# Optimization experiments

Hardware: AMD Instinct MI355X
Metric: run time of the kernel (lower is better)

The kernel has to match this reference:

```python
import jax, jax.numpy as jnp
import numpy as np

NEG_INF = -9e15
ALPHA = 0.2  # leaky relu negative slope


def setup_inputs() -> dict:
    key = jax.random.key(0)
    ks = jax.random.split(key, 7)
    B, N, FIN, FOUT = 4, 2048, 512, 128
    inp = {
        "input": jax.random.normal(ks[0], (B, N, FIN), dtype=jnp.float32),
        "W": jax.random.normal(ks[1], (FIN, FOUT), dtype=jnp.float32) * (1.414 / np.sqrt(FIN)),
        "a1": jax.random.normal(ks[2], (FOUT, 1), dtype=jnp.float32) * 0.1,
        "a2": jax.random.normal(ks[3], (FOUT, 1), dtype=jnp.float32) * 0.1,
        "adj": jax.random.randint(ks[4], (B, N, N), 0, 4, dtype=jnp.int32),
        "adj_tree": jax.random.randint(ks[5], (B, N, N), 0, 4, dtype=jnp.int32),
        "d1": 1,
        "d2": 2,
    }
    return inp


def reference(input, W, a1, a2, adj, adj_tree, d1, d2):
    # adj_tree is accepted but unused by the original forward.
    h = jnp.einsum("bnf,fo->bno", input, W)          # [B,N,out]
    t1 = jnp.einsum("bno,ok->bnk", h, a1)            # [B,N,1]
    t2 = jnp.einsum("bno,ok->bnk", h, a2)            # [B,N,1]
    # e[b,i,j] = t1[b,i] + t2[b,j]  (broadcast add, no repeat needed)
    e = jax.nn.leaky_relu(t1 + jnp.swapaxes(t2, 1, 2), negative_slope=ALPHA)
    att = jnp.where(adj == d1, e, NEG_INF)
    att = jnp.where(adj == d2, e, att)
    att = jax.nn.softmax(att, axis=2)
    # dropout is identity in eval mode (training=False)
    h_prime = jnp.einsum("bij,bjo->bio", att, h)     # [B,N,out]
    return h_prime
```

## Files before the change

kernel.cpp:

```cpp
#include <hip/hip_runtime.h>
#include <hip/hip_bf16.h>

#define NN 2048
#define FIN 512
#define FOUT 128
#define NEGV -9e15f
#define ALPHAV 0.2f
#define LOG2E 1.44269504088896340736f

typedef __attribute__((ext_vector_type(8))) short bf16x8;
typedef __attribute__((ext_vector_type(4))) float f32x4;

__device__ __forceinline__ unsigned cvt_pk_bf16(float lo, float hi) {
    unsigned r;
    asm("v_cvt_pk_bf16_f32 %0, %1, %2" : "=v"(r) : "v"(lo), "v"(hi));
    return r;
}

__device__ __forceinline__ unsigned short f32_to_bf16(float f) {
    unsigned int u = __float_as_uint(f);
    unsigned int r = (u + 0x7FFFu + ((u >> 16) & 1u)) >> 16;
    return (unsigned short)r;
}

__global__ void k_wrep(const float* __restrict__ W,
                       unsigned short* __restrict__ whi,
                       unsigned short* __restrict__ wlo) {
    int kt = blockIdx.x >> 3;
    int t_o = blockIdx.x & 7;
    int l = threadIdx.x;
    int lr = l & 15, lg = l >> 4;
    unsigned short vh[8], vl[8];
#pragma unroll
    for (int jj = 0; jj < 8; jj++) {
        float f = W[(size_t)(kt * 32 + lg * 8 + jj) * FOUT + t_o * 16 + lr];
        unsigned short h = f32_to_bf16(f);
        float hf = __uint_as_float(((unsigned)h) << 16);
        vh[jj] = h;
        vl[jj] = f32_to_bf16(f - hf);
    }
    size_t o = ((size_t)(kt * 8 + t_o) * 64 + l) * 8;
    *(uint4*)(whi + o) = *(const uint4*)vh;
    *(uint4*)(wlo + o) = *(const uint4*)vl;
}

__global__ void __launch_bounds__(256) k_h(const float* __restrict__ x,
                                           const unsigned short* __restrict__ whi,
                                           const unsigned short* __restrict__ wlo,
                                           const float* __restrict__ a1,
                                           const float* __restrict__ a2,
                                           unsigned short* __restrict__ hb,
                                           float* __restrict__ t1,
                                           float* __restrict__ t2) {
    __shared__ float lds_t1[4][16];
    __shared__ float lds_t2[4][16];
    int blk = blockIdx.x;
    int tid = threadIdx.x;
    int wv = tid >> 6, l = tid & 63;
    int lr = l & 15, lg = l >> 4;
    int row0 = blk * 16;

    const float* xp = x + (size_t)(row0 + lr) * FIN + lg * 8;
    const unsigned short* wb = whi + (size_t)(2 * wv) * 512 + l * 8;
    const unsigned short* lb = wlo + (size_t)(2 * wv) * 512 + l * 8;

    f32x4 acc0 = {0.f, 0.f, 0.f, 0.f};
    f32x4 acc1 = {0.f, 0.f, 0.f, 0.f};

#pragma unroll 2
    for (int kt = 0; kt < FIN / 32; kt++) {
        float4 xa = *(const float4*)(xp + kt * 32);
        float4 xb = *(const float4*)(xp + kt * 32 + 4);
        bf16x8 wh0 = *(const bf16x8*)(wb + (size_t)kt * 4096);
        bf16x8 wh1 = *(const bf16x8*)(wb + (size_t)kt * 4096 + 512);
        bf16x8 wl0 = *(const bf16x8*)(lb + (size_t)kt * 4096);
        bf16x8 wl1 = *(const bf16x8*)(lb + (size_t)kt * 4096 + 512);

        float f[8] = {xa.x, xa.y, xa.z, xa.w, xb.x, xb.y, xb.z, xb.w};
        unsigned uh[4], ul[4];
#pragma unroll
        for (int w = 0; w < 4; w++) {
            uh[w] = cvt_pk_bf16(f[2 * w], f[2 * w + 1]);
            float r0 = f[2 * w]     - __uint_as_float(uh[w] << 16);
            float r1 = f[2 * w + 1] - __uint_as_float(uh[w] & 0xffff0000u);
            ul[w] = cvt_pk_bf16(r0, r1);
        }
        bf16x8 xh = *(const bf16x8*)uh;
        bf16x8 xl = *(const bf16x8*)ul;

        acc0 = __builtin_amdgcn_mfma_f32_16x16x32_bf16(xh, wh0, acc0, 0, 0, 0);
        acc0 = __builtin_amdgcn_mfma_f32_16x16x32_bf16(xl, wh0, acc0, 0, 0, 0);
        acc0 = __builtin_amdgcn_mfma_f32_16x16x32_bf16(xh, wl0, acc0, 0, 0, 0);
        acc1 = __builtin_amdgcn_mfma_f32_16x16x32_bf16(xh, wh1, acc1, 0, 0, 0);
        acc1 = __builtin_amdgcn_mfma_f32_16x16x32_bf16(xl, wh1, acc1, 0, 0, 0);
        acc1 = __builtin_amdgcn_mfma_f32_16x16x32_bf16(xh, wl1, acc1, 0, 0, 0);
    }

    {
        float a10 = a1[(2 * wv) * 16 + lr], a11 = a1[(2 * wv + 1) * 16 + lr];
        float a20 = a2[(2 * wv) * 16 + lr], a21 = a2[(2 * wv + 1) * 16 + lr];
        float p1[4], p2[4];
#pragma unroll
        for (int r = 0; r < 4; r++) {
            p1[r] = acc0[r] * a10 + acc1[r] * a11;
            p2[r] = acc0[r] * a20 + acc1[r] * a21;
        }
#pragma unroll
        for (int off = 1; off < 16; off <<= 1) {
#pragma unroll
            for (int r = 0; r < 4; r++) {
                p1[r] += __shfl_xor(p1[r], off);
                p2[r] += __shfl_xor(p2[r], off);
            }
        }
        if (lr == 0) {
#pragma unroll
            for (int r = 0; r < 4; r++) {
                lds_t1[wv][lg * 4 + r] = p1[r];
                lds_t2[wv][lg * 4 + r] = p2[r];
            }
        }
        __syncthreads();
        if (tid < 16) {
            t1[row0 + tid] = (lds_t1[0][tid] + lds_t1[1][tid] + lds_t1[2][tid] + lds_t1[3][tid]) * LOG2E;
            t2[row0 + tid] = (lds_t2[0][tid] + lds_t2[1][tid] + lds_t2[2][tid] + lds_t2[3][tid]) * LOG2E;
        }
    }

    {
        size_t jtg = (size_t)(blk >> 1);
        int srcbase = (2 * (lg & 1)) * 16 + lr;
        bool active = (lg >> 1) == (blk & 1);
#pragma unroll
        for (int t = 0; t < 2; t++) {
            f32x4 a = t == 0 ? acc0 : acc1;
            unsigned p0 = cvt_pk_bf16(a[0], a[1]);
            unsigned p1 = cvt_pk_bf16(a[2], a[3]);
            unsigned g0 = __shfl((int)p0, srcbase);
            unsigned g1 = __shfl((int)p1, srcbase);
            unsigned g2 = __shfl((int)p0, srcbase + 16);
            unsigned g3 = __shfl((int)p1, srcbase + 16);
            if (active) {
                uint4 v = {g0, g1, g2, g3};
                int t_o = 2 * wv + t;
                *(uint4*)(hb + (jtg * 8 + t_o) * 512 + l * 8) = v;
            }
        }
    }
}

__global__ void __launch_bounds__(512, 4) k_attn(const int* __restrict__ adj,
                                                 const float* __restrict__ t1g,
                                                 const float* __restrict__ t2g,
                                                 const unsigned short* __restrict__ hb,
                                                 const int* __restrict__ d1p,
                                                 const int* __restrict__ d2p,
                                                 float* __restrict__ out) {
    __shared__ __align__(16) float accbuf[4][16][132];
    __shared__ float lds_s[8][16];
    __shared__ float lds_inv[16];

    int blk = blockIdx.x;
    int b = blk >> 7;
    int i0 = (blk & 127) * 16;
    int tid = threadIdx.x;
    int wv = tid >> 6;
    int l = tid & 63;
    int lr = l & 15, lg = l >> 4;
    int d1 = d1p[0], d2 = d2p[0];

    float t1v = t1g[b * NN + i0 + lr];
    const int* adjRow = adj + ((size_t)(b * NN + i0 + lr)) * NN + lg * 8;
    const float* t2p = t2g + b * NN + lg * 8;
    const unsigned short* hbbase = hb + (size_t)b * 64 * 4096 + (size_t)l * 8;

    float s = 0.f;
    f32x4 acc[8];
#pragma unroll
    for (int t = 0; t < 8; t++) acc[t] = (f32x4){0.f, 0.f, 0.f, 0.f};

#pragma unroll 2
    for (int jt = wv; jt < NN / 32; jt += 8) {
        int4 av0 = *(const int4*)(adjRow + jt * 32);
        int4 av1 = *(const int4*)(adjRow + jt * 32 + 4);
        float4 tb0 = *(const float4*)(t2p + jt * 32);
        float4 tb1 = *(const float4*)(t2p + jt * 32 + 4);
        bf16x8 hf[8];
#pragma unroll
        for (int t = 0; t < 8; t++)
            hf[t] = *(const bf16x8*)(hbbase + (size_t)jt * 4096 + t * 512);

        int ai[8] = {av0.x, av0.y, av0.z, av0.w, av1.x, av1.y, av1.z, av1.w};
        float tv[8] = {tb0.x, tb0.y, tb0.z, tb0.w, tb1.x, tb1.y, tb1.z, tb1.w};
        float p[8];
        float psum = 0.f;
#pragma unroll
        for (int jj = 0; jj < 8; jj++) {
            float v = t1v + tv[jj];
            float e = fmaxf(v, ALPHAV * v);
            float att = (ai[jj] == d1 || ai[jj] == d2) ? e : NEGV;
            p[jj] = __builtin_amdgcn_exp2f(att);
            psum += p[jj];
        }
        s += psum;

        unsigned u[4];
#pragma unroll
        for (int w = 0; w < 4; w++) u[w] = cvt_pk_bf16(p[2 * w], p[2 * w + 1]);
        bf16x8 pa = *(const bf16x8*)u;
#pragma unroll
        for (int t = 0; t < 8; t++)
            acc[t] = __builtin_amdgcn_mfma_f32_16x16x32_bf16(pa, hf[t], acc[t], 0, 0, 0);
    }

    s += __shfl_xor(s, 16);
    s += __shfl_xor(s, 32);
    if (l < 16) lds_s[wv][lr] = s;

    if (wv < 4) {
#pragma unroll
        for (int t = 0; t < 8; t++)
#pragma unroll
            for (int r = 0; r < 4; r++)
                accbuf[wv][lg * 4 + r][t * 16 + lr] = acc[t][r];
    }
    __syncthreads();
    if (wv >= 4) {
#pragma unroll
        for (int t = 0; t < 8; t++)
#pragma unroll
            for (int r = 0; r < 4; r++)
                accbuf[wv - 4][lg * 4 + r][t * 16 + lr] += acc[t][r];
    }
    if (tid < 16) {
        float st = 0.f;
#pragma unroll
        for (int w = 0; w < 8; w++) st += lds_s[w][tid];
        lds_inv[tid] = 1.0f / st;
    }
    __syncthreads();

    {
        int row = tid >> 5;
        int c4 = (tid & 31) * 4;
        float4 s0 = *(const float4*)&accbuf[0][row][c4];
        float4 s1 = *(const float4*)&accbuf[1][row][c4];
        float4 s2 = *(const float4*)&accbuf[2][row][c4];
        float4 s3 = *(const float4*)&accbuf[3][row][c4];
        float inv = lds_inv[row];
        float4 o;
        o.x = (s0.x + s1.x + s2.x + s3.x) * inv;
        o.y = (s0.y + s1.y + s2.y + s3.y) * inv;
        o.z = (s0.z + s1.z + s2.z + s3.z) * inv;
        o.w = (s0.w + s1.w + s2.w + s3.w) * inv;
        *(float4*)&out[((size_t)b * NN + i0 + row) * FOUT + c4] = o;
    }
}

extern "C" void kernel_launch(void* const* d_in, const int* in_sizes, int n_in,
                              void* d_out, int out_size, void* d_ws, size_t ws_size,
                              hipStream_t stream) {
    const float* x  = (const float*)d_in[0];
    const float* W  = (const float*)d_in[1];
    const float* a1 = (const float*)d_in[2];
    const float* a2 = (const float*)d_in[3];
    const int* adj  = (const int*)d_in[4];
    const int* d1p  = (const int*)d_in[6];
    const int* d2p  = (const int*)d_in[7];
    float* out = (float*)d_out;

    char* ws = (char*)d_ws;
    unsigned short* hbuf = (unsigned short*)(ws);
    float* t1            = (float*)(ws + 2u * 1024 * 1024);
    float* t2            = (float*)(ws + 2u * 1024 * 1024 + 32 * 1024);
    unsigned short* whi  = (unsigned short*)(ws + 2u * 1024 * 1024 + 64 * 1024);
    unsigned short* wlo  = (unsigned short*)(ws + 2u * 1024 * 1024 + 192 * 1024);

    k_wrep<<<dim3(128), dim3(64), 0, stream>>>(W, whi, wlo);
    k_h<<<dim3(512), dim3(256), 0, stream>>>(x, whi, wlo, a1, a2, hbuf, t1, t2);
    k_attn<<<dim3(512), dim3(512), 0, stream>>>(adj, t1, t2, hbuf, d1p, d2p, out);
}
```

Baseline: 47.27 us.

## Pack adjacency into bitmask in prep kernel, overlapped with h GEMM

Adds 2048 blocks to the h-projection kernel that read the int32 adjacency matrix and use wave ballots to build a per-row 1-bit mask of whether each entry equals d1 or d2, stored transposed for coalesced access. The attention kernel then reads 32-bit mask words instead of int adjacency rows and zeros masked probabilities after exp2. The adjacency matrix is still read once in full, but now that read runs alongside the GEMM blocks and the attention kernel's memory traffic and register load shrink. The cost is an extra mask write and read through the workspace.

```diff
diff --git a/kernel.cpp b/kernel.cpp
--- a/kernel.cpp
+++ b/kernel.cpp
@@ -44,20 +44,43 @@
     *(uint4*)(wlo + o) = *(const uint4*)vl;
 }
 
-__global__ void __launch_bounds__(256) k_h(const float* __restrict__ x,
-                                           const unsigned short* __restrict__ whi,
-                                           const unsigned short* __restrict__ wlo,
-                                           const float* __restrict__ a1,
-                                           const float* __restrict__ a2,
-                                           unsigned short* __restrict__ hb,
-                                           float* __restrict__ t1,
-                                           float* __restrict__ t2) {
+__global__ void __launch_bounds__(256) k_prep(const float* __restrict__ x,
+                                              const unsigned short* __restrict__ whi,
+                                              const unsigned short* __restrict__ wlo,
+                                              const float* __restrict__ a1,
+                                              const float* __restrict__ a2,
+                                              const int* __restrict__ adj,
+                                              const int* __restrict__ d1p,
+                                              const int* __restrict__ d2p,
+                                              unsigned short* __restrict__ hb,
+                                              float* __restrict__ t1,
+                                              float* __restrict__ t2,
+                                              unsigned* __restrict__ maskw) {
     __shared__ float lds_t1[4][16];
     __shared__ float lds_t2[4][16];
-    int blk = blockIdx.x;
     int tid = threadIdx.x;
     int wv = tid >> 6, l = tid & 63;
     int lr = l & 15, lg = l >> 4;
+
+    if (blockIdx.x < 2048) {
+        int d1 = d1p[0], d2 = d2p[0];
+        int row = blockIdx.x * 4 + wv;
+        int b = row >> 11, i = row & 2047;
+        const int* ap = adj + (size_t)row * NN + l;
+        unsigned* mbase = maskw + (size_t)b * 64 * NN + i;
+#pragma unroll 8
+        for (int k = 0; k < 32; k++) {
+            int a = ap[k * 64];
+            unsigned long long bal = __ballot(a == d1 || a == d2);
+            if (l == 0) {
+                mbase[(size_t)(2 * k) * NN]     = (unsigned)bal;
+                mbase[(size_t)(2 * k + 1) * NN] = (unsigned)(bal >> 32);
+            }
+        }
+        return;
+    }
+
+    int blk = blockIdx.x - 2048;
     int row0 = blk * 16;
 
     const float* xp = x + (size_t)(row0 + lr) * FIN + lg * 8;
@@ -149,12 +172,10 @@
     }
 }
 
-__global__ void __launch_bounds__(512, 4) k_attn(const int* __restrict__ adj,
+__global__ void __launch_bounds__(512, 4) k_attn(const unsigned* __restrict__ maskw,
                                                  const float* __restrict__ t1g,
                                                  const float* __restrict__ t2g,
                                                  const unsigned short* __restrict__ hb,
-                                                 const int* __restrict__ d1p,
-                                                 const int* __restrict__ d2p,
                                                  float* __restrict__ out) {
     __shared__ __align__(16) float accbuf[4][16][132];
     __shared__ float lds_s[8][16];
@@ -167,22 +188,25 @@
     int wv = tid >> 6;
     int l = tid & 63;
     int lr = l & 15, lg = l >> 4;
-    int d1 = d1p[0], d2 = d2p[0];
 
     float t1v = t1g[b * NN + i0 + lr];
-    const int* adjRow = adj + ((size_t)(b * NN + i0 + lr)) * NN + lg * 8;
     const float* t2p = t2g + b * NN + lg * 8;
     const unsigned short* hbbase = hb + (size_t)b * 64 * 4096 + (size_t)l * 8;
+    const unsigned* mrow = maskw + (size_t)b * 64 * NN + (i0 + lr);
+
+    unsigned mwv[8];
+#pragma unroll
+    for (int it = 0; it < 8; it++)
+        mwv[it] = mrow[(size_t)(wv + it * 8) * NN];
 
     float s = 0.f;
     f32x4 acc[8];
 #pragma unroll
     for (int t = 0; t < 8; t++) acc[t] = (f32x4){0.f, 0.f, 0.f, 0.f};
 
-#pragma unroll 2
-    for (int jt = wv; jt < NN / 32; jt += 8) {
-        int4 av0 = *(const int4*)(adjRow + jt * 32);
-        int4 av1 = *(const int4*)(adjRow + jt * 32 + 4);
+#pragma unroll
+    for (int it = 0; it < 8; it++) {
+        int jt = wv + it * 8;
         float4 tb0 = *(const float4*)(t2p + jt * 32);
         float4 tb1 = *(const float4*)(t2p + jt * 32 + 4);
         bf16x8 hf[8];
@@ -190,7 +214,7 @@
         for (int t = 0; t < 8; t++)
             hf[t] = *(const bf16x8*)(hbbase + (size_t)jt * 4096 + t * 512);
 
-        int ai[8] = {av0.x, av0.y, av0.z, av0.w, av1.x, av1.y, av1.z, av1.w};
+        unsigned mbyte = mwv[it] >> (lg * 8);
         float tv[8] = {tb0.x, tb0.y, tb0.z, tb0.w, tb1.x, tb1.y, tb1.z, tb1.w};
         float p[8];
         float psum = 0.f;
@@ -198,8 +222,8 @@
         for (int jj = 0; jj < 8; jj++) {
             float v = t1v + tv[jj];
             float e = fmaxf(v, ALPHAV * v);
-            float att = (ai[jj] == d1 || ai[jj] == d2) ? e : NEGV;
-            p[jj] = __builtin_amdgcn_exp2f(att);
+            float ex = __builtin_amdgcn_exp2f(e);
+            p[jj] = (mbyte & (1u << jj)) ? ex : 0.f;
             psum += p[jj];
         }
         s += psum;
@@ -275,8 +299,10 @@
     float* t2            = (float*)(ws + 2u * 1024 * 1024 + 32 * 1024);
     unsigned short* whi  = (unsigned short*)(ws + 2u * 1024 * 1024 + 64 * 1024);
     unsigned short* wlo  = (unsigned short*)(ws + 2u * 1024 * 1024 + 192 * 1024);
+    unsigned* maskw      = (unsigned*)(ws + 2u * 1024 * 1024 + 320 * 1024);
 
     k_wrep<<<dim3(128), dim3(64), 0, stream>>>(W, whi, wlo);
-    k_h<<<dim3(512), dim3(256), 0, stream>>>(x, whi, wlo, a1, a2, hbuf, t1, t2);
-    k_attn<<<dim3(512), dim3(512), 0, stream>>>(adj, t1, t2, hbuf, d1p, d2p, out);
-}
+    k_prep<<<dim3(2560), dim3(256), 0, stream>>>(x, whi, wlo, a1, a2, adj, d1p, d2p,
+                                                 hbuf, t1, t2, maskw);
+    k_attn<<<dim3(512), dim3(512), 0, stream>>>(maskw, t1, t2, hbuf, out);
+}
```

Measured after the change: 69.64 us. 47.3% more time.
